# Performance work log

Hardware: AMD Instinct MI355X
Metric: run time of the kernel (lower is better)

## Reference

```python
import jax, jax.numpy as jnp
import numpy as np
import math

B, T, D, V, M = 32, 2048, 512, 4096, 64
COVERAGE_FLOOR = 0.05
BIG = 1e30


def masked_median(values, mask):
    # values, mask: [B, T]; torch.median = lower median = sorted[(n-1)//2]
    valid = mask > 0.5
    n = valid.sum(axis=1)  # [B]
    s = jnp.sort(jnp.where(valid, values, BIG), axis=1)
    idx = jnp.maximum((n - 1) // 2, 0)
    med = jnp.take_along_axis(s, idx[:, None], axis=1)  # [B,1]
    return jnp.where(n[:, None] > 0, med, 0.0)


def masked_mean(values, mask):
    # values: [B,T,D], mask: [B,T]
    denom = jnp.maximum(mask.sum(axis=1, keepdims=True), 1.0)  # [B,1]
    return (values * mask[:, :, None]).sum(axis=1) / denom


def masked_std(values, mask, mean):
    denom = jnp.maximum(mask.sum(axis=1, keepdims=True), 1.0)
    diff2 = (values - mean[:, None, :]) ** 2 * mask[:, :, None]
    return jnp.sqrt(diff2.sum(axis=1) / jnp.maximum(denom, 1e-6) + 1e-6)


def conv1d(x, w, b):
    # x: [B,T,D], w: [K=3, I=D, O=D], padding=1 -> same length
    y = jax.lax.conv_general_dilated(x, w, window_strides=(1,), padding=[(1, 1)],
                                     dimension_numbers=('NHC', 'HIO', 'NHC'))
    return y + b


def layer_norm(x, w, b, eps=1e-5):
    mu = x.mean(axis=-1, keepdims=True)
    var = ((x - mu) ** 2).mean(axis=-1, keepdims=True)
    return (x - mu) * jax.lax.rsqrt(var + eps) * w + b


def setup_inputs() -> dict:
    key = jax.random.key(0)
    ks = jax.random.split(key, 20)
    units = jax.random.randint(ks[0], (B, T), 0, V)
    dur = jax.random.uniform(ks[1], (B, T), jnp.float32, 0.01, 2.0)
    valid = (jax.random.uniform(ks[2], (B, T)) > 0.1).astype(jnp.float32)
    speech = valid * (jax.random.uniform(ks[3], (B, T)) > 0.2).astype(jnp.float32)
    s = 0.02
    params = dict(
        emb=jax.random.normal(ks[4], (V, D)) * s,
        W_in=jax.random.normal(ks[5], (D + 2, D)) * s, b_in=jnp.zeros((D,)),
        W_c1=jax.random.normal(ks[6], (3, D, D)) * s, b_c1=jnp.zeros((D,)),
        W_c2=jax.random.normal(ks[7], (3, D, D)) * s, b_c2=jnp.zeros((D,)),
        ln_w=jnp.ones((D,)), ln_b=jnp.zeros((D,)),
        codebook_key=jax.random.normal(ks[8], (M, D)) * s,
        W_p1=jax.random.normal(ks[9], (2 * D, D)) * s, b_p1=jnp.zeros((D,)),
        W_p2=jax.random.normal(ks[10], (D, D)) * s, b_p2=jnp.zeros((D,)),
    )
    return dict(prompt_content_units=units, prompt_duration_obs=dur,
                prompt_valid_mask=valid, prompt_speech_mask=speech, **params)


def reference(prompt_content_units, prompt_duration_obs, prompt_valid_mask, prompt_speech_mask,
              emb, W_in, b_in, W_c1, b_c1, W_c2, b_c2, ln_w, ln_b,
              codebook_key, W_p1, b_p1, W_p2, b_p2):
    valid = jnp.clip(prompt_valid_mask, 0.0, 1.0)          # [B,T]
    speech = jnp.clip(prompt_speech_mask, 0.0, 1.0) * valid
    logdur = jnp.log(jnp.maximum(prompt_duration_obs, 1e-4)) * valid
    global_rate = masked_median(logdur, speech)             # [B,1]
    ref_residual = (logdur - global_rate) * valid            # [B,T]

    # encode prompt summary
    sil_flag = jnp.maximum(valid - speech, 0.0)
    h = jnp.concatenate([emb[prompt_content_units],
                         ref_residual[:, :, None], sil_flag[:, :, None]], axis=-1)
    h = h @ W_in + b_in                                      # [B,T,D]
    h = jax.nn.gelu(conv1d(h, W_c1, b_c1), approximate=False)
    h = jax.nn.gelu(conv1d(h, W_c2, b_c2), approximate=False)
    h = layer_norm(h, ln_w, ln_b) * valid[:, :, None]

    summary_mask = speech  # summary_pool_speech_only=True
    mean = masked_mean(h, summary_mask)                      # [B,D]
    std = masked_std(h, summary_mask, mean)                  # [B,D]
    z = jnp.concatenate([mean, std], axis=-1) @ W_p1 + b_p1
    summary_state = jnp.tanh(jax.nn.gelu(z, approximate=False) @ W_p2 + b_p2)
    support_raw = valid.sum(axis=1, keepdims=True)           # [B,1]
    support = jnp.maximum(support_raw, 1.0)
    summary_state = jnp.where(support_raw > 0.0, summary_state, 0.0)

    score = jnp.einsum('btd,md->btm', h, codebook_key) / math.sqrt(float(D))
    score = jnp.where(valid[:, :, None] <= 0.0, -10000.0, score)
    attn = jax.nn.softmax(score, axis=-1) * valid[:, :, None]  # [B,T,M]
    role_mass = attn.sum(axis=1)                               # [B,M]
    role_denom = jnp.maximum(role_mass, 1e-6)
    role_value = jnp.einsum('btm,bt->bm', attn, ref_residual) / role_denom
    diff2 = (ref_residual[:, :, None] - role_value[:, None, :]) ** 2  # [B,T,M]
    role_var = (attn * diff2).sum(axis=1) / role_denom
    role_var = jnp.maximum(jnp.where(role_mass > 0.0, role_var, 1e-4), 1e-4)
    role_coverage = jnp.maximum(role_mass / support, COVERAGE_FLOOR)
    prompt_role_fit = jnp.einsum('btm,bm->bt', attn, role_value) * valid

    return (global_rate, summary_state, role_value, role_var, role_coverage, prompt_role_fit)
```

## Files before the change

### kernel.cpp

```cpp
#include <hip/hip_runtime.h>
#include <hip/hip_bf16.h>
#include <math.h>


typedef unsigned short u16;
typedef unsigned char u8;
typedef __attribute__((ext_vector_type(8))) short short8;
typedef __attribute__((ext_vector_type(4))) float f32x4;
typedef __attribute__((ext_vector_type(4))) int int4v;
typedef __attribute__((ext_vector_type(8))) int int8v;

constexpr int B_ = 32, T_ = 2048, D_ = 512, V_ = 4096, M_ = 64, TP_ = 2050;

constexpr int OUT_GR = 0;
constexpr int OUT_SUM = 32;
constexpr int OUT_RV = 16416;
constexpr int OUT_VAR = 18464;
constexpr int OUT_COV = 20512;
constexpr int OUT_FIT = 22560;

constexpr size_t OFF_S0 = 0;
constexpr size_t OFF_S1 = OFF_S0 + 2048 * 4;
constexpr size_t OFF_S2 = OFF_S1 + 2048 * 4;
constexpr size_t OFF_SH = OFF_S2 + 2048 * 4;
constexpr size_t OFF_SH2 = OFF_SH + 16384 * 4;
constexpr size_t ZERO_BYTES = OFF_SH2 + 16384 * 4;
constexpr size_t OFF_RESID = ZERO_BYTES;
constexpr size_t OFF_GR = OFF_RESID + 65536 * 4;
constexpr size_t OFF_SUP = OFF_GR + 128;
constexpr size_t OFF_SPC = OFF_SUP + 128;
constexpr size_t OFF_RVW = OFF_SPC + 128;
constexpr size_t OFF_WTIN = OFF_RVW + 8192;
constexpr size_t OFF_WTC1 = OFF_WTIN + 524288;
constexpr size_t OFF_WTC2 = OFF_WTC1 + 786432;
constexpr size_t OFF_CKB = OFF_WTC2 + 786432;
constexpr size_t OFF_EMBB = OFF_CKB + 65536;
constexpr size_t OFF_TBL = OFF_EMBB + 4194304;
constexpr size_t OFF_H0 = OFF_TBL + 8388608;
constexpr size_t OFF_H1 = OFF_H0 + 33587200;
constexpr size_t OFF_H2 = OFF_H1 + 33587200;
constexpr size_t OFF_ATTN = OFF_H2 + 67108864;

__device__ __forceinline__ float clamp01(float x) { return fminf(fmaxf(x, 0.f), 1.f); }
__device__ __forceinline__ float b2f(u16 u) { return __uint_as_float(((unsigned)u) << 16); }
__device__ __forceinline__ u16 f2b(float f) {
  unsigned u = __float_as_uint(f);
  unsigned r = (u + 0x7FFFu + ((u >> 16) & 1u)) >> 16;
  return (u16)r;
}
__device__ __forceinline__ u8 f2fp8(float f) {
  return (u8)(__builtin_amdgcn_cvt_pk_fp8_f32(f, f, 0, false) & 0xFF);
}
__device__ __forceinline__ float gelu_f(float x) {
  return 0.5f * x * (1.0f + erff(x * 0.7071067811865475f));
}
__device__ __forceinline__ void gload16(const void* g, void* l) {
  __builtin_amdgcn_global_load_lds((const __attribute__((address_space(1))) void*)g,
                                   (__attribute__((address_space(3))) void*)l, 16, 0, 0);
}

__global__ __launch_bounds__(256) void median_kernel(
    const float* __restrict__ dur, const float* __restrict__ vmask,
    const float* __restrict__ smask, float* __restrict__ out0,
    float* __restrict__ gr, float* __restrict__ sup, float* __restrict__ spc,
    float* __restrict__ resid) {
  int b = blockIdx.x, tid = threadIdx.x;
  int wv = tid >> 6, lane = tid & 63;
  __shared__ float wredf[8];
  __shared__ int wredi[4];
  unsigned keys[8];
  float ldv[8], vmv[8];
  float vs = 0.f, ss = 0.f;
#pragma unroll
  for (int j = 0; j < 8; ++j) {
    int t = j * 256 + tid;
    float vm = clamp01(vmask[b * T_ + t]);
    float sm = clamp01(smask[b * T_ + t]) * vm;
    vs += vm; ss += sm;
    float ld = logf(fmaxf(dur[b * T_ + t], 1e-4f)) * vm;
    ldv[j] = ld; vmv[j] = vm;
    unsigned bits = __float_as_uint(ld);
    unsigned key = (bits & 0x80000000u) ? ~bits : (bits | 0x80000000u);
    keys[j] = (sm > 0.5f) ? key : 0xFFFFFFFFu;
  }
  for (int o = 32; o > 0; o >>= 1) { vs += __shfl_xor(vs, o); ss += __shfl_xor(ss, o); }
  if (lane == 0) { wredf[wv] = vs; wredf[4 + wv] = ss; }
  __syncthreads();
  float s_sup = wredf[0] + wredf[1] + wredf[2] + wredf[3];
  float s_spc = wredf[4] + wredf[5] + wredf[6] + wredf[7];
  int n = (int)(s_spc + 0.5f);
  int target = (n > 0) ? ((n - 1) / 2 + 1) : 1;
  unsigned lo = 0u, hi = 0xFFFFFFFFu;
  for (int it = 0; it < 32; ++it) {
    unsigned mid = lo + ((hi - lo) >> 1);
    int c = 0;
#pragma unroll
    for (int j = 0; j < 8; ++j) c += (keys[j] <= mid) ? 1 : 0;
    for (int o = 32; o > 0; o >>= 1) c += __shfl_xor(c, o);
    __syncthreads();
    if (lane == 0) wredi[wv] = c;
    __syncthreads();
    int tot = wredi[0] + wredi[1] + wredi[2] + wredi[3];
    if (tot >= target) hi = mid; else lo = mid + 1;
  }
  float med = 0.f;
  if (n > 0) {
    unsigned K = lo;
    unsigned ub = (K & 0x80000000u) ? (K & 0x7FFFFFFFu) : ~K;
    med = __uint_as_float(ub);
  }
  if (tid == 0) { out0[OUT_GR + b] = med; gr[b] = med; sup[b] = s_sup; spc[b] = s_spc; }
#pragma unroll
  for (int j = 0; j < 8; ++j) {
    int t = j * 256 + tid;
    resid[b * T_ + t] = (ldv[j] - med) * vmv[j];
  }
}

__global__ __launch_bounds__(256) void wpack_kernel(
    const float* __restrict__ W_in, const float* __restrict__ W_c1,
    const float* __restrict__ W_c2, u16* __restrict__ wtin,
    u8* __restrict__ wtc1, u8* __restrict__ wtc2) {
  __shared__ float tile[64][65];
  int x = blockIdx.x;
  int m = x >> 6, tl = x & 63;
  int kt = tl >> 3, nt = tl & 7;
  const float* src;
  if (m == 0) src = W_in;
  else if (m <= 3) src = W_c1 + (size_t)(m - 1) * 262144;
  else src = W_c2 + (size_t)(m - 4) * 262144;
  int tid = threadIdx.x;
#pragma unroll
  for (int j = 0; j < 16; ++j) {
    int idx = j * 256 + tid;
    int r = idx >> 6, c = idx & 63;
    tile[r][c] = src[(size_t)(kt * 64 + r) * 512 + nt * 64 + c];
  }
  __syncthreads();
  if (m == 0) {
#pragma unroll
    for (int j = 0; j < 16; ++j) {
      int idx = j * 256 + tid;
      int r = idx >> 6, c = idx & 63;
      wtin[(size_t)(nt * 64 + r) * 512 + kt * 64 + c] = f2b(tile[c][r]);
    }
  } else {
    u8* dst = (m <= 3) ? wtc1 + (size_t)(m - 1) * 262144
                       : wtc2 + (size_t)(m - 4) * 262144;
#pragma unroll
    for (int j = 0; j < 16; ++j) {
      int idx = j * 256 + tid;
      int r = idx >> 6, c = idx & 63;
      dst[(size_t)(nt * 64 + r) * 512 + kt * 64 + c] = f2fp8(tile[c][r] * 64.f);
    }
  }
}

__global__ __launch_bounds__(256) void convert_kernel(
    const float* __restrict__ ck, const float* __restrict__ emb,
    u16* __restrict__ ckb, u16* __restrict__ embb) {
  int idx = blockIdx.x * 256 + threadIdx.x;
  float4 v;
  u16* dst;
  if (idx < 8192) {
    v = reinterpret_cast<const float4*>(ck)[idx];
    dst = ckb + idx * 4;
  } else {
    int i = idx - 8192;
    v = reinterpret_cast<const float4*>(emb)[i];
    dst = embb + (size_t)i * 4;
  }
  uint2 o;
  o.x = (unsigned)f2b(v.x) | ((unsigned)f2b(v.y) << 16);
  o.y = (unsigned)f2b(v.z) | ((unsigned)f2b(v.w) << 16);
  *reinterpret_cast<uint2*>(dst) = o;
}

__global__ __launch_bounds__(256) void gemm_plain_kernel(
    const u16* __restrict__ A, const u16* __restrict__ Bt,
    const float* __restrict__ bias, u16* __restrict__ Cout) {
  __shared__ u16 ldsA[64 * 64];
  __shared__ u16 ldsB[128 * 64];
  const int tid = threadIdx.x;
  const int row0 = blockIdx.x * 64;
  const int col0 = blockIdx.y * 128;

  f32x4 acc[2][4] = {};
  const int wv = tid >> 6, lane = tid & 63;
  const int wr = (wv >> 1) << 5;
  const int wc = (wv & 1) << 6;
  const int lr = lane & 15, cgrp = lane >> 4;

  const u16* Ab = A + (size_t)row0 * 512;
  const u16* Bb = Bt + (size_t)col0 * 512;
  for (int k0 = 0; k0 < 512; k0 += 64) {
    if (k0) __syncthreads();
#pragma unroll
    for (int j = 0; j < 2; ++j) {
      int ci = j * 256 + tid;
      int r = ci >> 3, s = ci & 7;
      int gs = s ^ (r & 7);
      gload16(Ab + (size_t)r * 512 + k0 + gs * 8, &ldsA[ci * 8]);
    }
#pragma unroll
    for (int j = 0; j < 4; ++j) {
      int ci = j * 256 + tid;
      int r = ci >> 3, s = ci & 7;
      int gs = s ^ (r & 7);
      gload16(Bb + (size_t)r * 512 + k0 + gs * 8, &ldsB[ci * 8]);
    }
    __syncthreads();
#pragma unroll
    for (int kk = 0; kk < 2; ++kk) {
      short8 af[2], bfr[4];
#pragma unroll
      for (int m = 0; m < 2; ++m) {
        int r = wr + m * 16 + lr;
        int s = (kk * 4 + cgrp) ^ (r & 7);
        af[m] = *reinterpret_cast<const short8*>(&ldsA[(r << 6) + (s << 3)]);
      }
#pragma unroll
      for (int n = 0; n < 4; ++n) {
        int r = wc + n * 16 + lr;
        int s = (kk * 4 + cgrp) ^ (r & 7);
        bfr[n] = *reinterpret_cast<const short8*>(&ldsB[(r << 6) + (s << 3)]);
      }
#pragma unroll
      for (int m = 0; m < 2; ++m)
#pragma unroll
        for (int n = 0; n < 4; ++n)
          acc[m][n] = __builtin_amdgcn_mfma_f32_16x16x32_bf16(af[m], bfr[n], acc[m][n], 0, 0, 0);
    }
  }
#pragma unroll
  for (int m = 0; m < 2; ++m)
#pragma unroll
    for (int n = 0; n < 4; ++n)
#pragma unroll
      for (int r = 0; r < 4; ++r) {
        int lrow = wr + m * 16 + (lane >> 4) * 4 + r;
        int lcol = wc + n * 16 + (lane & 15);
        Cout[(size_t)(row0 + lrow) * 512 + col0 + lcol] =
            f2b(acc[m][n][r] + bias[col0 + lcol]);
      }
}

template <int PADOUT, int OUTFP8>
__global__ __launch_bounds__(256, 3) void conv_gemm_kernel(
    const u8* __restrict__ A, const u8* __restrict__ Bt,
    const float* __restrict__ bias, void* __restrict__ Cout) {
  __shared__ u8 ldsA[130 * 128];
  __shared__ u8 ldsB[3 * 64 * 128];
  const int tid = threadIdx.x;
  const int id = blockIdx.x;
  const int wg = (id & 7) * 512 + (id >> 3);
  const int rb = wg >> 3, cb = wg & 7;
  const int row0 = rb * 128, col0 = cb * 64;
  const int b = row0 >> 11, t0 = row0 & 2047;
  const size_t aBase = ((size_t)b * TP_ + t0) * 512;
  const size_t oBase = PADOUT ? ((size_t)b * TP_ + 1 + t0) : (size_t)row0;

  f32x4 acc[4][2] = {};
  const int wv = tid >> 6, lane = tid & 63;
  const int wr = (wv >> 1) << 6;
  const int wc = (wv & 1) << 5;
  const int lr = lane & 15, cgrp = lane >> 4;

  const u8* Ab = A + aBase;
#pragma unroll 1
  for (int k0 = 0; k0 < 512; k0 += 128) {
    if (k0) __syncthreads();
#pragma unroll
    for (int j = 0; j < 5; ++j) {
      int ci = j * 256 + tid;
      if (ci < 1040) {
        int r = ci >> 3, s = ci & 7;
        int gs = s ^ (r & 7);
        gload16(Ab + (size_t)r * 512 + k0 + gs * 16, &ldsA[ci * 16]);
      }
    }
#pragma unroll
    for (int j = 0; j < 6; ++j) {
      int ci = j * 256 + tid;
      int r = ci >> 3, s = ci & 7;
      int tap = r >> 6, n = r & 63;
      int gs = s ^ (r & 7);
      gload16(Bt + ((size_t)(tap * 512 + col0 + n)) * 512 + k0 + gs * 16, &ldsB[ci * 16]);
    }
    __syncthreads();
#pragma unroll
    for (int tap = 0; tap < 3; ++tap) {
      int8v af[4], bfr[2];
#pragma unroll
      for (int m = 0; m < 4; ++m) {
        int r = wr + m * 16 + lr + tap;
        int s0 = (2 * cgrp) ^ (r & 7);
        int s1 = (2 * cgrp + 1) ^ (r & 7);
        int4v lo = *reinterpret_cast<const int4v*>(&ldsA[(r << 7) + (s0 << 4)]);
        int4v hi = *reinterpret_cast<const int4v*>(&ldsA[(r << 7) + (s1 << 4)]);
        af[m] = __builtin_shufflevector(lo, hi, 0, 1, 2, 3, 4, 5, 6, 7);
      }
#pragma unroll
      for (int n = 0; n < 2; ++n) {
        int rB = tap * 64 + wc + n * 16 + lr;
        int s0 = (2 * cgrp) ^ (rB & 7);
        int s1 = (2 * cgrp + 1) ^ (rB & 7);
        int4v lo = *reinterpret_cast<const int4v*>(&ldsB[(rB << 7) + (s0 << 4)]);
        int4v hi = *reinterpret_cast<const int4v*>(&ldsB[(rB << 7) + (s1 << 4)]);
        bfr[n] = __builtin_shufflevector(lo, hi, 0, 1, 2, 3, 4, 5, 6, 7);
      }
#pragma unroll
      for (int m = 0; m < 4; ++m)
#pragma unroll
        for (int n = 0; n < 2; ++n)
          acc[m][n] = __builtin_amdgcn_mfma_scale_f32_16x16x128_f8f6f4(
              af[m], bfr[n], acc[m][n], 0, 0, 0, 0x7F7F7F7F, 0, 0x7F7F7F7F);
    }
  }
#pragma unroll
  for (int m = 0; m < 4; ++m)
#pragma unroll
    for (int n = 0; n < 2; ++n)
#pragma unroll
      for (int r = 0; r < 4; ++r) {
        int lrow = wr + m * 16 + (lane >> 4) * 4 + r;
        int lcol = wc + n * 16 + (lane & 15);
        float v = acc[m][n][r] * (1.f / 4096.f) + bias[col0 + lcol];
        v = gelu_f(v);
        if (OUTFP8)
          ((u8*)Cout)[(oBase + lrow) * 512 + col0 + lcol] = f2fp8(v * 64.f);
        else
          ((u16*)Cout)[(oBase + lrow) * 512 + col0 + lcol] = f2b(v);
      }
}

__global__ __launch_bounds__(256) void gather_kernel(
    const int* __restrict__ units, const float* __restrict__ resid,
    const float* __restrict__ vmask, const float* __restrict__ smask,
    const u16* __restrict__ tbl, const float* __restrict__ w512,
    const float* __restrict__ w513, u8* __restrict__ h0p, u8* __restrict__ h1p) {
  int row = blockIdx.x * 4 + (threadIdx.x >> 6);
  int b = row / TP_, tp = row - b * TP_;
  int lane = threadIdx.x & 63;
  size_t o = (size_t)row * 512 + lane * 8;
  if (tp == 0 || tp == TP_ - 1) {
    uint2 z = {0, 0};
    *reinterpret_cast<uint2*>(&h0p[o]) = z;
    *reinterpret_cast<uint2*>(&h1p[o]) = z;
    return;
  }
  int t = tp - 1, g = b * T_ + t;
  float vm = clamp01(vmask[g]);
  float sm = clamp01(smask[g]) * vm;
  float sil = fmaxf(vm - sm, 0.f);
  float rs = resid[g];
  int u = units[g];
  uint4 tv = *reinterpret_cast<const uint4*>(tbl + (size_t)u * 512 + lane * 8);
  float tr[8];
  tr[0] = __uint_as_float(tv.x << 16); tr[1] = __uint_as_float(tv.x & 0xFFFF0000u);
  tr[2] = __uint_as_float(tv.y << 16); tr[3] = __uint_as_float(tv.y & 0xFFFF0000u);
  tr[4] = __uint_as_float(tv.z << 16); tr[5] = __uint_as_float(tv.z & 0xFFFF0000u);
  tr[6] = __uint_as_float(tv.w << 16); tr[7] = __uint_as_float(tv.w & 0xFFFF0000u);
  const float* a = w512 + lane * 8;
  const float* c = w513 + lane * 8;
  float f[8];
#pragma unroll
  for (int j = 0; j < 8; ++j) f[j] = (tr[j] + rs * a[j] + sil * c[j]) * 64.f;
  unsigned lo = __builtin_amdgcn_cvt_pk_fp8_f32(f[0], f[1], 0, false);
  lo = __builtin_amdgcn_cvt_pk_fp8_f32(f[2], f[3], lo, true);
  unsigned hi = __builtin_amdgcn_cvt_pk_fp8_f32(f[4], f[5], 0, false);
  hi = __builtin_amdgcn_cvt_pk_fp8_f32(f[6], f[7], hi, true);
  uint2 val = {lo, hi};
  *reinterpret_cast<uint2*>(&h0p[o]) = val;
}

__global__ __launch_bounds__(256) void lnpool_kernel(
    u16* __restrict__ h, const float* __restrict__ lnw,
    const float* __restrict__ lnb, const float* __restrict__ vmask,
    const float* __restrict__ smask, float* __restrict__ Sh,
    float* __restrict__ Sh2) {
  int b = blockIdx.y, chunk = blockIdx.x, tid = threadIdx.x;
  int lane = tid & 63, tof = tid >> 6;
  __shared__ float shA[512], shQ[512];
  shA[tid] = 0.f; shA[tid + 256] = 0.f;
  shQ[tid] = 0.f; shQ[tid + 256] = 0.f;
  __syncthreads();
  int d8 = lane * 8;
  float wv_[8], bv_[8];
#pragma unroll
  for (int j = 0; j < 8; ++j) { wv_[j] = lnw[d8 + j]; bv_[j] = lnb[d8 + j]; }
  float a[8] = {}, q[8] = {};
  for (int i = 0; i < 32; ++i) {
    int t = chunk * 128 + i * 4 + tof;
    int g = b * T_ + t;
    float vm = clamp01(vmask[g]);
    float sp = clamp01(smask[g]) * vm;
    u16* p = h + (size_t)g * 512 + d8;
    uint4 raw = *reinterpret_cast<const uint4*>(p);
    float x[8];
    x[0] = __uint_as_float(raw.x << 16); x[1] = __uint_as_float(raw.x & 0xFFFF0000u);
    x[2] = __uint_as_float(raw.y << 16); x[3] = __uint_as_float(raw.y & 0xFFFF0000u);
    x[4] = __uint_as_float(raw.z << 16); x[5] = __uint_as_float(raw.z & 0xFFFF0000u);
    x[6] = __uint_as_float(raw.w << 16); x[7] = __uint_as_float(raw.w & 0xFFFF0000u);
    float s = 0.f, sq = 0.f;
#pragma unroll
    for (int j = 0; j < 8; ++j) { s += x[j]; sq = fmaf(x[j], x[j], sq); }
    for (int o = 32; o > 0; o >>= 1) { s += __shfl_xor(s, o); sq += __shfl_xor(sq, o); }
    float mu = s * (1.f / 512.f);
    float var = fmaxf(sq * (1.f / 512.f) - mu * mu, 0.f);
    float rstd = rsqrtf(var + 1e-5f);
    u16 ob[8];
#pragma unroll
    for (int j = 0; j < 8; ++j) {
      float y = (x[j] - mu) * rstd * wv_[j] + bv_[j];
      ob[j] = f2b(y * vm);
      float yr = b2f(ob[j]);
      a[j] = fmaf(yr, sp, a[j]);
      q[j] = fmaf(yr * yr, sp, q[j]);
    }
    uint4 val;
    val.x = (unsigned)ob[0] | ((unsigned)ob[1] << 16);
    val.y = (unsigned)ob[2] | ((unsigned)ob[3] << 16);
    val.z = (unsigned)ob[4] | ((unsigned)ob[5] << 16);
    val.w = (unsigned)ob[6] | ((unsigned)ob[7] << 16);
    *reinterpret_cast<uint4*>(p) = val;
  }
#pragma unroll
  for (int j = 0; j < 8; ++j) {
    atomicAdd(&shA[d8 + j], a[j]);
    atomicAdd(&shQ[d8 + j], q[j]);
  }
  __syncthreads();
  atomicAdd(&Sh[b * 512 + tid], shA[tid]);
  atomicAdd(&Sh[b * 512 + tid + 256], shA[tid + 256]);
  atomicAdd(&Sh2[b * 512 + tid], shQ[tid]);
  atomicAdd(&Sh2[b * 512 + tid + 256], shQ[tid + 256]);
}

__global__ __launch_bounds__(256) void score_kernel(
    const u16* __restrict__ h, const u16* __restrict__ ckb,
    const float* __restrict__ resid, const float* __restrict__ vmask,
    float* __restrict__ attn, float* __restrict__ S0, float* __restrict__ S1,
    float* __restrict__ S2) {
  __shared__ char smem[98304];
  __shared__ float s0s[64], s1s[64], s2s[64];
  u16* ckl = (u16*)smem;
  u16* ldsH = (u16*)(smem + 65536);
  float* attn_lds = (float*)smem;

  const int tid = threadIdx.x;
  const int base = blockIdx.x * 256;
  const int bq = base >> 11;

#pragma unroll
  for (int it = 0; it < 16; ++it) {
    int ci = it * 256 + tid;
    int m = ci >> 6, s = ci & 63;
    int sw = (s & 56) | ((s & 7) ^ (m & 7));
    *reinterpret_cast<uint4*>(&ckl[(m << 9) + (sw << 3)]) =
        *reinterpret_cast<const uint4*>(&ckb[(m << 9) + (s << 3)]);
  }
  if (tid < 64) { s0s[tid] = 0.f; s1s[tid] = 0.f; s2s[tid] = 0.f; }

  const int wv = tid >> 6, lane = tid & 63;
  const int lr = lane & 15, cgrp = lane >> 4;
  const int hi = lane >> 4, lf = lane & 15;
  f32x4 acc[4][4] = {};

  const u16* hb = h + (size_t)base * 512;
  for (int k0 = 0; k0 < 512; k0 += 64) {
    __syncthreads();
#pragma unroll
    for (int j = 0; j < 8; ++j) {
      int ci = j * 256 + tid;
      int r = ci >> 3, s = ci & 7;
      int gs = s ^ (r & 7);
      gload16(hb + (size_t)r * 512 + k0 + gs * 8, &ldsH[ci * 8]);
    }
    __syncthreads();
#pragma unroll
    for (int kk = 0; kk < 2; ++kk) {
      short8 af[4], bfr[4];
#pragma unroll
      for (int m = 0; m < 4; ++m) {
        int r = wv * 64 + m * 16 + lr;
        int s = (kk * 4 + cgrp) ^ (r & 7);
        af[m] = *reinterpret_cast<const short8*>(&ldsH[(r << 6) + (s << 3)]);
      }
#pragma unroll
      for (int n = 0; n < 4; ++n) {
        int r = n * 16 + lr;
        int s = (kk * 4 + cgrp) ^ (r & 7);
        bfr[n] = *reinterpret_cast<const short8*>(&ckl[(r << 9) + k0 + (s << 3)]);
      }
#pragma unroll
      for (int m = 0; m < 4; ++m)
#pragma unroll
        for (int n = 0; n < 4; ++n)
          acc[m][n] = __builtin_amdgcn_mfma_f32_16x16x32_bf16(af[m], bfr[n], acc[m][n], 0, 0, 0);
    }
  }
  __syncthreads();

  const float scale = 0.04419417382415922f;
  float s0p[4] = {0.f, 0.f, 0.f, 0.f};
  float s1p[4] = {0.f, 0.f, 0.f, 0.f};
  float s2p[4] = {0.f, 0.f, 0.f, 0.f};
#pragma unroll
  for (int m = 0; m < 4; ++m) {
#pragma unroll
    for (int rr = 0; rr < 4; ++rr) {
      int tl = wv * 64 + m * 16 + hi * 4 + rr;
      int tg = base + tl;
      float v[4];
#pragma unroll
      for (int n = 0; n < 4; ++n) v[n] = acc[m][n][rr] * scale;
      float mx = fmaxf(fmaxf(v[0], v[1]), fmaxf(v[2], v[3]));
      mx = fmaxf(mx, __shfl_xor(mx, 1));
      mx = fmaxf(mx, __shfl_xor(mx, 2));
      mx = fmaxf(mx, __shfl_xor(mx, 4));
      mx = fmaxf(mx, __shfl_xor(mx, 8));
      float e[4], sum = 0.f;
#pragma unroll
      for (int n = 0; n < 4; ++n) { e[n] = expf(v[n] - mx); sum += e[n]; }
      sum += __shfl_xor(sum, 1);
      sum += __shfl_xor(sum, 2);
      sum += __shfl_xor(sum, 4);
      sum += __shfl_xor(sum, 8);
      float vm = clamp01(vmask[tg]);
      float inv = vm / sum;
      float rs = resid[tg];
#pragma unroll
      for (int n = 0; n < 4; ++n) {
        float a = e[n] * inv;
        attn_lds[tl * 65 + n * 16 + lf] = a;
        s0p[n] += a; s1p[n] += a * rs; s2p[n] += a * rs * rs;
      }
    }
  }
#pragma unroll
  for (int n = 0; n < 4; ++n) {
    s0p[n] += __shfl_xor(s0p[n], 16); s0p[n] += __shfl_xor(s0p[n], 32);
    s1p[n] += __shfl_xor(s1p[n], 16); s1p[n] += __shfl_xor(s1p[n], 32);
    s2p[n] += __shfl_xor(s2p[n], 16); s2p[n] += __shfl_xor(s2p[n], 32);
  }
  if (hi == 0) {
#pragma unroll
    for (int n = 0; n < 4; ++n) {
      atomicAdd(&s0s[n * 16 + lf], s0p[n]);
      atomicAdd(&s1s[n * 16 + lf], s1p[n]);
      atomicAdd(&s2s[n * 16 + lf], s2p[n]);
    }
  }
  __syncthreads();
#pragma unroll
  for (int it = 0; it < 16; ++it) {
    int ci = it * 256 + tid;
    int tl = ci >> 4, c4 = (ci & 15) * 4;
    float4 val;
    val.x = attn_lds[tl * 65 + c4];
    val.y = attn_lds[tl * 65 + c4 + 1];
    val.z = attn_lds[tl * 65 + c4 + 2];
    val.w = attn_lds[tl * 65 + c4 + 3];
    *reinterpret_cast<float4*>(&attn[(size_t)(base + tl) * 64 + c4]) = val;
  }
  if (tid < 64) {
    atomicAdd(&S0[bq * 64 + tid], s0s[tid]);
    atomicAdd(&S1[bq * 64 + tid], s1s[tid]);
    atomicAdd(&S2[bq * 64 + tid], s2s[tid]);
  }
}

__global__ __launch_bounds__(64) void role_kernel(
    const float* __restrict__ S0, const float* __restrict__ S1,
    const float* __restrict__ S2, const float* __restrict__ sup,
    float* __restrict__ out, float* __restrict__ rv) {
  int b = blockIdx.x, m = threadIdx.x;
  float mass = S0[b * 64 + m], s1 = S1[b * 64 + m], s2 = S2[b * 64 + m];
  float dn = fmaxf(mass, 1e-6f);
  float v = s1 / dn;
  float var = (s2 - 2.f * v * s1 + v * v * mass) / dn;
  var = fmaxf(var, 1e-4f);
  float support = fmaxf(sup[b], 1.f);
  float cov = fmaxf(mass / support, 0.05f);
  out[OUT_RV + b * 64 + m] = v;
  out[OUT_VAR + b * 64 + m] = var;
  out[OUT_COV + b * 64 + m] = cov;
  rv[b * 64 + m] = v;
}

__global__ __launch_bounds__(512) void mlp_kernel(
    const float* __restrict__ Sh, const float* __restrict__ Sh2,
    const float* __restrict__ spc, const float* __restrict__ sup,
    const float* __restrict__ Wp1, const float* __restrict__ bp1,
    const float* __restrict__ Wp2, const float* __restrict__ bp2,
    float* __restrict__ out) {
  int b = blockIdx.x, j = threadIdx.x;
  __shared__ float ms[1024];
  __shared__ float zg[512];
  float denom = fmaxf(spc[b], 1.0f);
  float mean = Sh[b * 512 + j] / denom;
  float ex2 = Sh2[b * 512 + j] / denom;
  float var = fmaxf(ex2 - mean * mean, 0.f);
  ms[j] = mean;
  ms[512 + j] = sqrtf(var + 1e-6f);
  __syncthreads();
  float z = bp1[j];
  for (int k = 0; k < 1024; ++k) z = fmaf(ms[k], Wp1[k * 512 + j], z);
  zg[j] = gelu_f(z);
  __syncthreads();
  float o = bp2[j];
  for (int k = 0; k < 512; ++k) o = fmaf(zg[k], Wp2[k * 512 + j], o);
  float sm = tanhf(o);
  out[OUT_SUM + b * 512 + j] = (sup[b] > 0.f) ? sm : 0.f;
}

__global__ __launch_bounds__(256) void fit_kernel(
    const float* __restrict__ attn, const float* __restrict__ rv,
    const float* __restrict__ vmask, float* __restrict__ out) {
  int tid = threadIdx.x;
  int wv = tid >> 6, lane = tid & 63;
  int t = blockIdx.x * 4 + wv;
  int b = t >> 11;
  float a = attn[(size_t)t * 64 + lane] * rv[b * 64 + lane];
  for (int o = 32; o > 0; o >>= 1) a += __shfl_xor(a, o);
  if (lane == 0) out[OUT_FIT + t] = a * clamp01(vmask[t]);
}

extern "C" void kernel_launch(void* const* d_in, const int* in_sizes, int n_in,
                              void* d_out, int out_size, void* d_ws, size_t ws_size,
                              hipStream_t stream) {
  (void)in_sizes; (void)n_in; (void)out_size; (void)ws_size;
  const int* units = (const int*)d_in[0];
  const float* dur = (const float*)d_in[1];
  const float* vmask = (const float*)d_in[2];
  const float* smask = (const float*)d_in[3];
  const float* emb = (const float*)d_in[4];
  const float* W_in = (const float*)d_in[5];
  const float* b_in = (const float*)d_in[6];
  const float* W_c1 = (const float*)d_in[7];
  const float* b_c1 = (const float*)d_in[8];
  const float* W_c2 = (const float*)d_in[9];
  const float* b_c2 = (const float*)d_in[10];
  const float* ln_w = (const float*)d_in[11];
  const float* ln_b = (const float*)d_in[12];
  const float* ck = (const float*)d_in[13];
  const float* W_p1 = (const float*)d_in[14];
  const float* b_p1 = (const float*)d_in[15];
  const float* W_p2 = (const float*)d_in[16];
  const float* b_p2 = (const float*)d_in[17];
  float* out = (float*)d_out;

  char* w = (char*)d_ws;
  float* S0 = (float*)(w + OFF_S0);
  float* S1 = (float*)(w + OFF_S1);
  float* S2 = (float*)(w + OFF_S2);
  float* Sh = (float*)(w + OFF_SH);
  float* Sh2 = (float*)(w + OFF_SH2);
  float* resid = (float*)(w + OFF_RESID);
  float* gr = (float*)(w + OFF_GR);
  float* sup = (float*)(w + OFF_SUP);
  float* spc = (float*)(w + OFF_SPC);
  float* rv = (float*)(w + OFF_RVW);
  u16* wtin = (u16*)(w + OFF_WTIN);
  u8* wtc1 = (u8*)(w + OFF_WTC1);
  u8* wtc2 = (u8*)(w + OFF_WTC2);
  u16* ckb = (u16*)(w + OFF_CKB);
  u16* embb = (u16*)(w + OFF_EMBB);
  u16* tbl = (u16*)(w + OFF_TBL);
  u8* h0p = (u8*)(w + OFF_H0);
  u8* h1p = (u8*)(w + OFF_H1);
  u16* h2 = (u16*)(w + OFF_H2);
  float* attn = (float*)(w + OFF_ATTN);

  hipMemsetAsync(d_ws, 0, ZERO_BYTES, stream);
  median_kernel<<<B_, 256, 0, stream>>>(dur, vmask, smask, out, gr, sup, spc, resid);
  wpack_kernel<<<448, 256, 0, stream>>>(W_in, W_c1, W_c2, wtin, wtc1, wtc2);
  convert_kernel<<<2080, 256, 0, stream>>>(ck, emb, ckb, embb);
  gemm_plain_kernel<<<dim3(64, 4), 256, 0, stream>>>(embb, wtin, b_in, tbl);
  gather_kernel<<<B_ * TP_ / 4, 256, 0, stream>>>(units, resid, vmask, smask, tbl,
                                                  W_in + 512 * 512, W_in + 513 * 512, h0p, h1p);
  conv_gemm_kernel<1, 1><<<4096, 256, 0, stream>>>(h0p, wtc1, b_c1, (void*)h1p);
  conv_gemm_kernel<0, 0><<<4096, 256, 0, stream>>>(h1p, wtc2, b_c2, (void*)h2);
  lnpool_kernel<<<dim3(16, 32), 256, 0, stream>>>(h2, ln_w, ln_b, vmask, smask, Sh, Sh2);
  score_kernel<<<256, 256, 0, stream>>>(h2, ckb, resid, vmask, attn, S0, S1, S2);
  role_kernel<<<B_, 64, 0, stream>>>(S0, S1, S2, sup, out, rv);
  mlp_kernel<<<B_, 512, 0, stream>>>(Sh, Sh2, spc, sup, W_p1, b_p1, W_p2, b_p2, out);
  fit_kernel<<<B_ * T_ / 4, 256, 0, stream>>>(attn, rv, vmask, out);
}
```

Measured before the change: 298.6 us.

## Store conv2 output and attention in narrower formats to cut memory traffic

```diff
diff --git a/kernel.cpp b/kernel.cpp
--- a/kernel.cpp
+++ b/kernel.cpp
@@ -245,10 +245,10 @@
       }
 }
 
-template <int PADOUT, int OUTFP8>
+template <int PADOUT>
 __global__ __launch_bounds__(256, 3) void conv_gemm_kernel(
     const u8* __restrict__ A, const u8* __restrict__ Bt,
-    const float* __restrict__ bias, void* __restrict__ Cout) {
+    const float* __restrict__ bias, u8* __restrict__ Cout) {
   __shared__ u8 ldsA[130 * 128];
   __shared__ u8 ldsB[3 * 64 * 128];
   const int tid = threadIdx.x;
@@ -327,10 +327,7 @@
         int lcol = wc + n * 16 + (lane & 15);
         float v = acc[m][n][r] * (1.f / 4096.f) + bias[col0 + lcol];
         v = gelu_f(v);
-        if (OUTFP8)
-          ((u8*)Cout)[(oBase + lrow) * 512 + col0 + lcol] = f2fp8(v * 64.f);
-        else
-          ((u16*)Cout)[(oBase + lrow) * 512 + col0 + lcol] = f2b(v);
+        Cout[(oBase + lrow) * 512 + col0 + lcol] = f2fp8(v * 64.f);
       }
 }
 
@@ -375,10 +372,10 @@
 }
 
 __global__ __launch_bounds__(256) void lnpool_kernel(
-    u16* __restrict__ h, const float* __restrict__ lnw,
-    const float* __restrict__ lnb, const float* __restrict__ vmask,
-    const float* __restrict__ smask, float* __restrict__ Sh,
-    float* __restrict__ Sh2) {
+    const u8* __restrict__ hin, u16* __restrict__ hout,
+    const float* __restrict__ lnw, const float* __restrict__ lnb,
+    const float* __restrict__ vmask, const float* __restrict__ smask,
+    float* __restrict__ Sh, float* __restrict__ Sh2) {
   int b = blockIdx.y, chunk = blockIdx.x, tid = threadIdx.x;
   int lane = tid & 63, tof = tid >> 6;
   __shared__ float shA[512], shQ[512];
@@ -390,18 +387,23 @@
 #pragma unroll
   for (int j = 0; j < 8; ++j) { wv_[j] = lnw[d8 + j]; bv_[j] = lnb[d8 + j]; }
   float a[8] = {}, q[8] = {};
+  const float inv64 = 1.f / 64.f;
   for (int i = 0; i < 32; ++i) {
     int t = chunk * 128 + i * 4 + tof;
     int g = b * T_ + t;
     float vm = clamp01(vmask[g]);
     float sp = clamp01(smask[g]) * vm;
-    u16* p = h + (size_t)g * 512 + d8;
-    uint4 raw = *reinterpret_cast<const uint4*>(p);
+    const u8* p = hin + (size_t)g * 512 + d8;
+    uint2 raw = *reinterpret_cast<const uint2*>(p);
     float x[8];
-    x[0] = __uint_as_float(raw.x << 16); x[1] = __uint_as_float(raw.x & 0xFFFF0000u);
-    x[2] = __uint_as_float(raw.y << 16); x[3] = __uint_as_float(raw.y & 0xFFFF0000u);
-    x[4] = __uint_as_float(raw.z << 16); x[5] = __uint_as_float(raw.z & 0xFFFF0000u);
-    x[6] = __uint_as_float(raw.w << 16); x[7] = __uint_as_float(raw.w & 0xFFFF0000u);
+    x[0] = __builtin_amdgcn_cvt_f32_fp8(raw.x, 0) * inv64;
+    x[1] = __builtin_amdgcn_cvt_f32_fp8(raw.x, 1) * inv64;
+    x[2] = __builtin_amdgcn_cvt_f32_fp8(raw.x, 2) * inv64;
+    x[3] = __builtin_amdgcn_cvt_f32_fp8(raw.x, 3) * inv64;
+    x[4] = __builtin_amdgcn_cvt_f32_fp8(raw.y, 0) * inv64;
+    x[5] = __builtin_amdgcn_cvt_f32_fp8(raw.y, 1) * inv64;
+    x[6] = __builtin_amdgcn_cvt_f32_fp8(raw.y, 2) * inv64;
+    x[7] = __builtin_amdgcn_cvt_f32_fp8(raw.y, 3) * inv64;
     float s = 0.f, sq = 0.f;
 #pragma unroll
     for (int j = 0; j < 8; ++j) { s += x[j]; sq = fmaf(x[j], x[j], sq); }
@@ -412,18 +414,17 @@
     u16 ob[8];
 #pragma unroll
     for (int j = 0; j < 8; ++j) {
-      float y = (x[j] - mu) * rstd * wv_[j] + bv_[j];
-      ob[j] = f2b(y * vm);
-      float yr = b2f(ob[j]);
-      a[j] = fmaf(yr, sp, a[j]);
-      q[j] = fmaf(yr * yr, sp, q[j]);
+      float y = ((x[j] - mu) * rstd * wv_[j] + bv_[j]) * vm;
+      ob[j] = f2b(y);
+      a[j] = fmaf(y, sp, a[j]);
+      q[j] = fmaf(y * y, sp, q[j]);
     }
     uint4 val;
     val.x = (unsigned)ob[0] | ((unsigned)ob[1] << 16);
     val.y = (unsigned)ob[2] | ((unsigned)ob[3] << 16);
     val.z = (unsigned)ob[4] | ((unsigned)ob[5] << 16);
     val.w = (unsigned)ob[6] | ((unsigned)ob[7] << 16);
-    *reinterpret_cast<uint4*>(p) = val;
+    *reinterpret_cast<uint4*>(&hout[(size_t)g * 512 + d8]) = val;
   }
 #pragma unroll
   for (int j = 0; j < 8; ++j) {
@@ -440,7 +441,7 @@
 __global__ __launch_bounds__(256) void score_kernel(
     const u16* __restrict__ h, const u16* __restrict__ ckb,
     const float* __restrict__ resid, const float* __restrict__ vmask,
-    float* __restrict__ attn, float* __restrict__ S0, float* __restrict__ S1,
+    u16* __restrict__ attn, float* __restrict__ S0, float* __restrict__ S1,
     float* __restrict__ S2) {
   __shared__ char smem[98304];
   __shared__ float s0s[64], s1s[64], s2s[64];
@@ -532,9 +533,9 @@
       float rs = resid[tg];
 #pragma unroll
       for (int n = 0; n < 4; ++n) {
-        float a = e[n] * inv;
-        attn_lds[tl * 65 + n * 16 + lf] = a;
-        s0p[n] += a; s1p[n] += a * rs; s2p[n] += a * rs * rs;
+        float aa = e[n] * inv;
+        attn_lds[tl * 65 + n * 16 + lf] = aa;
+        s0p[n] += aa; s1p[n] += aa * rs; s2p[n] += aa * rs * rs;
       }
     }
   }
@@ -554,15 +555,18 @@
   }
   __syncthreads();
 #pragma unroll
-  for (int it = 0; it < 16; ++it) {
+  for (int it = 0; it < 8; ++it) {
     int ci = it * 256 + tid;
-    int tl = ci >> 4, c4 = (ci & 15) * 4;
-    float4 val;
-    val.x = attn_lds[tl * 65 + c4];
-    val.y = attn_lds[tl * 65 + c4 + 1];
-    val.z = attn_lds[tl * 65 + c4 + 2];
-    val.w = attn_lds[tl * 65 + c4 + 3];
-    *reinterpret_cast<float4*>(&attn[(size_t)(base + tl) * 64 + c4]) = val;
+    int tl = ci >> 3, c8 = (ci & 7) * 8;
+    u16 ob[8];
+#pragma unroll
+    for (int j = 0; j < 8; ++j) ob[j] = f2b(attn_lds[tl * 65 + c8 + j]);
+    uint4 val;
+    val.x = (unsigned)ob[0] | ((unsigned)ob[1] << 16);
+    val.y = (unsigned)ob[2] | ((unsigned)ob[3] << 16);
+    val.z = (unsigned)ob[4] | ((unsigned)ob[5] << 16);
+    val.w = (unsigned)ob[6] | ((unsigned)ob[7] << 16);
+    *reinterpret_cast<uint4*>(&attn[(size_t)(base + tl) * 64 + c8]) = val;
   }
   if (tid < 64) {
     atomicAdd(&S0[bq * 64 + tid], s0s[tid]);
@@ -605,24 +609,36 @@
   ms[j] = mean;
   ms[512 + j] = sqrtf(var + 1e-6f);
   __syncthreads();
-  float z = bp1[j];
-  for (int k = 0; k < 1024; ++k) z = fmaf(ms[k], Wp1[k * 512 + j], z);
+  float z0 = 0.f, z1 = 0.f, z2 = 0.f, z3 = 0.f;
+  for (int k = 0; k < 1024; k += 4) {
+    z0 = fmaf(ms[k], Wp1[(size_t)k * 512 + j], z0);
+    z1 = fmaf(ms[k + 1], Wp1[(size_t)(k + 1) * 512 + j], z1);
+    z2 = fmaf(ms[k + 2], Wp1[(size_t)(k + 2) * 512 + j], z2);
+    z3 = fmaf(ms[k + 3], Wp1[(size_t)(k + 3) * 512 + j], z3);
+  }
+  float z = bp1[j] + ((z0 + z1) + (z2 + z3));
   zg[j] = gelu_f(z);
   __syncthreads();
-  float o = bp2[j];
-  for (int k = 0; k < 512; ++k) o = fmaf(zg[k], Wp2[k * 512 + j], o);
+  float o0 = 0.f, o1 = 0.f, o2 = 0.f, o3 = 0.f;
+  for (int k = 0; k < 512; k += 4) {
+    o0 = fmaf(zg[k], Wp2[(size_t)k * 512 + j], o0);
+    o1 = fmaf(zg[k + 1], Wp2[(size_t)(k + 1) * 512 + j], o1);
+    o2 = fmaf(zg[k + 2], Wp2[(size_t)(k + 2) * 512 + j], o2);
+    o3 = fmaf(zg[k + 3], Wp2[(size_t)(k + 3) * 512 + j], o3);
+  }
+  float o = bp2[j] + ((o0 + o1) + (o2 + o3));
   float sm = tanhf(o);
   out[OUT_SUM + b * 512 + j] = (sup[b] > 0.f) ? sm : 0.f;
 }
 
 __global__ __launch_bounds__(256) void fit_kernel(
-    const float* __restrict__ attn, const float* __restrict__ rv,
+    const u16* __restrict__ attn, const float* __restrict__ rv,
     const float* __restrict__ vmask, float* __restrict__ out) {
   int tid = threadIdx.x;
   int wv = tid >> 6, lane = tid & 63;
   int t = blockIdx.x * 4 + wv;
   int b = t >> 11;
-  float a = attn[(size_t)t * 64 + lane] * rv[b * 64 + lane];
+  float a = b2f(attn[(size_t)t * 64 + lane]) * rv[b * 64 + lane];
   for (int o = 32; o > 0; o >>= 1) a += __shfl_xor(a, o);
   if (lane == 0) out[OUT_FIT + t] = a * clamp01(vmask[t]);
 }
@@ -670,8 +686,9 @@
   u16* tbl = (u16*)(w + OFF_TBL);
   u8* h0p = (u8*)(w + OFF_H0);
   u8* h1p = (u8*)(w + OFF_H1);
-  u16* h2 = (u16*)(w + OFF_H2);
-  float* attn = (float*)(w + OFF_ATTN);
+  u8* h2f = (u8*)(w + OFF_H2);
+  u16* h2b = (u16*)(w + OFF_H0);
+  u16* attn = (u16*)(w + OFF_ATTN);
 
   hipMemsetAsync(d_ws, 0, ZERO_BYTES, stream);
   median_kernel<<<B_, 256, 0, stream>>>(dur, vmask, smask, out, gr, sup, spc, resid);
@@ -680,10 +697,10 @@
   gemm_plain_kernel<<<dim3(64, 4), 256, 0, stream>>>(embb, wtin, b_in, tbl);
   gather_kernel<<<B_ * TP_ / 4, 256, 0, stream>>>(units, resid, vmask, smask, tbl,
                                                   W_in + 512 * 512, W_in + 513 * 512, h0p, h1p);
-  conv_gemm_kernel<1, 1><<<4096, 256, 0, stream>>>(h0p, wtc1, b_c1, (void*)h1p);
-  conv_gemm_kernel<0, 0><<<4096, 256, 0, stream>>>(h1p, wtc2, b_c2, (void*)h2);
-  lnpool_kernel<<<dim3(16, 32), 256, 0, stream>>>(h2, ln_w, ln_b, vmask, smask, Sh, Sh2);
-  score_kernel<<<256, 256, 0, stream>>>(h2, ckb, resid, vmask, attn, S0, S1, S2);
+  conv_gemm_kernel<1><<<4096, 256, 0, stream>>>(h0p, wtc1, b_c1, h1p);
+  conv_gemm_kernel<0><<<4096, 256, 0, stream>>>(h1p, wtc2, b_c2, h2f);
+  lnpool_kernel<<<dim3(16, 32), 256, 0, stream>>>(h2f, h2b, ln_w, ln_b, vmask, smask, Sh, Sh2);
+  score_kernel<<<256, 256, 0, stream>>>(h2b, ckb, resid, vmask, attn, S0, S1, S2);
   role_kernel<<<B_, 64, 0, stream>>>(S0, S1, S2, sup, out, rv);
   mlp_kernel<<<B_, 512, 0, stream>>>(Sh, Sh2, spc, sup, W_p1, b_p1, W_p2, b_p2, out);
   fit_kernel<<<B_ * T_ / 4, 256, 0, stream>>>(attn, rv, vmask, out);
```

Measured after the change: 304.0 us. About the same (+1.8%).
